# Kernel optimization log

Hardware: AMD Instinct MI355X
Metric: run time of the kernel (lower is better)

## Reference

```python
import jax, jax.numpy as jnp
import numpy as np

N, E, F_IN, HID, G = 20000, 320000, 128, 128, 64
H, D = 8, 32  # TransformerConv heads, per-head dim


def setup_inputs() -> dict:
    key = jax.random.key(0)
    ks = jax.random.split(key, 24)
    def w(k, i, o):
        return (jax.random.normal(k, (i, o), jnp.float32) / np.float32(np.sqrt(i)))
    def b(k, o):
        return jax.random.normal(k, (o,), jnp.float32) * 0.01
    inp = {
        'x': jax.random.normal(ks[0], (N, F_IN), jnp.float32),
        'edge_index': jax.random.randint(ks[1], (2, E), 0, N, jnp.int32),
        'batch': jnp.sort(jax.random.randint(ks[2], (N,), 0, G, jnp.int32)),
        # SAGEConv 1: 128 -> 128 (lin_l has bias, lin_r none)
        's1_wl': w(ks[3], 128, 128), 's1_bl': b(ks[4], 128), 's1_wr': w(ks[5], 128, 128),
        # SAGEConv 2: 128 -> 256
        's2_wl': w(ks[6], 128, 256), 's2_bl': b(ks[7], 256), 's2_wr': w(ks[8], 128, 256),
        # TransformerConv 1: 256 -> 8*32
        't1_wq': w(ks[9], 256, 256), 't1_bq': b(ks[10], 256),
        't1_wk': w(ks[11], 256, 256), 't1_bk': b(ks[12], 256),
        't1_wv': w(ks[13], 256, 256), 't1_bv': b(ks[14], 256),
        't1_ws': w(ks[15], 256, 256), 't1_bs': b(ks[16], 256),
        # TransformerConv 2
        't2_wq': w(ks[17], 256, 256), 't2_bq': b(ks[18], 256),
        't2_wk': w(ks[19], 256, 256), 't2_bk': b(ks[20], 256),
        't2_wv': w(ks[21], 256, 256), 't2_bv': b(ks[22], 256),
        't2_ws': w(ks[23], 256, 256), 't2_bs': b(jax.random.fold_in(key, 100), 256),
        # proj MLP: 256 -> 512 -> HID
        'p1_w': w(jax.random.fold_in(key, 101), 256, 512), 'p1_b': b(jax.random.fold_in(key, 102), 512),
        'p2_w': w(jax.random.fold_in(key, 103), 512, HID), 'p2_b': b(jax.random.fold_in(key, 104), HID),
    }
    return inp


def _sage(x, src, dst, wl, bl, wr):
    # PyG SAGEConv (aggr='mean'): lin_l(mean_j x_j) + lin_r(x_i)
    s = jax.ops.segment_sum(x[src], dst, num_segments=N)           # [N,F]
    cnt = jax.ops.segment_sum(jnp.ones((src.shape[0], 1), x.dtype), dst, num_segments=N)
    mean = s / jnp.maximum(cnt, 1.0)
    return mean @ wl + bl + x @ wr


def _tconv(x, src, dst, wq, bq, wk, bk, wv, bv, ws, bs):
    # PyG TransformerConv(256, 32, heads=8): per-edge attention + skip
    q = (x @ wq + bq).reshape(N, H, D)
    k = (x @ wk + bk).reshape(N, H, D)
    v = (x @ wv + bv).reshape(N, H, D)
    logits = jnp.einsum('ehd,ehd->eh', q[dst], k[src]) / np.float32(np.sqrt(D))  # [E,H]
    m = jax.ops.segment_max(logits, dst, num_segments=N)           # [N,H]
    p = jnp.exp(logits - m[dst])
    denom = jax.ops.segment_sum(p, dst, num_segments=N)
    p = p / denom[dst]                                              # softmax per target node per head
    agg = jax.ops.segment_sum(p[:, :, None] * v[src], dst, num_segments=N)  # [N,H,D]
    return agg.reshape(N, H * D) + x @ ws + bs


def reference(x, edge_index, batch, s1_wl, s1_bl, s1_wr, s2_wl, s2_bl, s2_wr,
              t1_wq, t1_bq, t1_wk, t1_bk, t1_wv, t1_bv, t1_ws, t1_bs,
              t2_wq, t2_bq, t2_wk, t2_bk, t2_wv, t2_bv, t2_ws, t2_bs,
              p1_w, p1_b, p2_w, p2_b):
    src, dst = edge_index[0], edge_index[1]
    h = jax.nn.relu(_sage(x, src, dst, s1_wl, s1_bl, s1_wr))
    h = jax.nn.relu(_sage(h, src, dst, s2_wl, s2_bl, s2_wr))
    h = jax.nn.relu(_tconv(h, src, dst, t1_wq, t1_bq, t1_wk, t1_bk, t1_wv, t1_bv, t1_ws, t1_bs))
    h = jax.nn.relu(_tconv(h, src, dst, t2_wq, t2_bq, t2_wk, t2_bk, t2_wv, t2_bv, t2_ws, t2_bs))
    # proj: ReLU -> Linear(256,512) -> ReLU -> Linear(512,HID) -> Sigmoid
    h = jax.nn.relu(h)
    h = jax.nn.relu(h @ p1_w + p1_b)
    h = jax.nn.sigmoid(h @ p2_w + p2_b)
    return jax.ops.segment_max(h, batch, num_segments=G)            # global_max_pool [G,HID]
```

## Files before the change

### kernel.cpp

```cpp
#include <hip/hip_runtime.h>
#include <hip/hip_bf16.h>
#include <hip/hip_fp16.h>
#include <math.h>

#define NN 20000
#define EE 320000
#define GG 64
#define CH 16

typedef __hip_bfloat16 bf16;
typedef __attribute__((ext_vector_type(8))) short short8;
typedef __attribute__((ext_vector_type(4))) float f32x4;
typedef __attribute__((ext_vector_type(4))) unsigned int uint4v;
typedef __attribute__((ext_vector_type(2))) _Float16 half2v;
typedef unsigned int uint;
typedef unsigned short ushort;

__device__ __forceinline__ float bfr2f(ushort u) {
    union { uint i; float f; } c; c.i = ((uint)u) << 16; return c.f;
}
__device__ __forceinline__ ushort f2bfr(float f) {
    bf16 h = __float2bfloat16(f);
    return *(ushort*)&h;
}

__device__ __forceinline__ float dot2acc(uint a, uint b, float c) {
#if __has_builtin(__builtin_amdgcn_fdot2)
    return __builtin_amdgcn_fdot2(__builtin_bit_cast(half2v, a),
                                  __builtin_bit_cast(half2v, b), c, false);
#else
    half2v ha = __builtin_bit_cast(half2v, a);
    half2v hb = __builtin_bit_cast(half2v, b);
    return c + (float)ha.x * (float)hb.x + (float)ha.y * (float)hb.y;
#endif
}

__device__ __forceinline__ void load_lds16(const void* g, void* l) {
    __builtin_amdgcn_global_load_lds(
        (const __attribute__((address_space(1))) unsigned int*)g,
        (__attribute__((address_space(3))) unsigned int*)l, 16, 0, 0);
}

#define PREP_CONV  10000
#define PREP_TP    (PREP_CONV + 800)
#define PREP_BIAS  (PREP_TP + 8)
#define PREP_OUTZ  (PREP_BIAS + 32)
#define PREP_COUNT (PREP_OUTZ + 1250)

__global__ __launch_bounds__(256) void prep_kernel(
    const float* x, bf16* xm1,
    const float* s1_wr, const float* s1_wl, const float* s2_wr, const float* s2_wl,
    const float* t1_wq, const float* t1_wk, const float* t1_wv, const float* t1_ws,
    const float* t2_wq, const float* t2_wk, const float* t2_wv, const float* t2_ws,
    const float* p1_w, const float* p2_w,
    bf16* w1cat, bf16* w2cat, bf16* qw1, bf16* qw2, bf16* p1t, bf16* p2t,
    const float* b1q, const float* b1k, const float* b1v, const float* b1s,
    const float* b2q, const float* b2k, const float* b2v, const float* b2s,
    float* qb1, float* qb2,
    float* pool_out,
    const int* dst, int* cnt) {
    __shared__ float tile[32][33];
    int bid = blockIdx.x;
    int tid = threadIdx.x;
    if (bid < PREP_CONV) {
        int i = bid * 256 + tid;
        int r = i >> 7, c = i & 127;
        xm1[(size_t)r * 256 + c] = __float2bfloat16(x[i]);
    } else if (bid < PREP_TP) {
        int tb = bid - PREP_CONV;
        const float* W; bf16* Wt; int KW, NW, KT, KO, lt;
        const float* t1w[4] = {t1_wq, t1_wk, t1_wv, t1_ws};
        const float* t2w[4] = {t2_wq, t2_wk, t2_wv, t2_ws};
        if (tb < 16)       { W = s1_wr; Wt = w1cat; KW = 128; NW = 128; KT = 256; KO = 0;   lt = tb; }
        else if (tb < 32)  { W = s1_wl; Wt = w1cat; KW = 128; NW = 128; KT = 256; KO = 128; lt = tb - 16; }
        else if (tb < 64)  { W = s2_wr; Wt = w2cat; KW = 128; NW = 256; KT = 256; KO = 0;   lt = tb - 32; }
        else if (tb < 96)  { W = s2_wl; Wt = w2cat; KW = 128; NW = 256; KT = 256; KO = 128; lt = tb - 64; }
        else if (tb < 352) { int m = (tb - 96) >> 6;  W = t1w[m]; Wt = qw1 + m * 65536; KW = 256; NW = 256; KT = 256; KO = 0; lt = (tb - 96) & 63; }
        else if (tb < 608) { int m = (tb - 352) >> 6; W = t2w[m]; Wt = qw2 + m * 65536; KW = 256; NW = 256; KT = 256; KO = 0; lt = (tb - 352) & 63; }
        else if (tb < 736) { W = p1_w; Wt = p1t; KW = 256; NW = 512; KT = 256; KO = 0; lt = tb - 608; }
        else               { W = p2_w; Wt = p2t; KW = 512; NW = 128; KT = 512; KO = 0; lt = tb - 736; }
        int ntiles_n = NW >> 5;
        int k0 = (lt / ntiles_n) * 32;
        int n0 = (lt % ntiles_n) * 32;
        int tx = tid & 31, ty = tid >> 5;
        #pragma unroll
        for (int r = 0; r < 4; r++)
            tile[ty + 8 * r][tx] = W[(size_t)(k0 + ty + 8 * r) * NW + n0 + tx];
        __syncthreads();
        #pragma unroll
        for (int r = 0; r < 4; r++)
            Wt[(size_t)(n0 + ty + 8 * r) * KT + KO + k0 + tx] =
                __float2bfloat16(tile[tx][ty + 8 * r]);
    } else if (bid < PREP_BIAS) {
        int i = (bid - PREP_TP) * 256 + tid;
        if (i < 2048) {
            float* d = (i < 1024) ? qb1 : qb2;
            int j = i & 1023;
            const float* s;
            if (i < 1024) s = (j < 256) ? b1q : (j < 512) ? b1k : (j < 768) ? b1v : b1s;
            else          s = (j < 256) ? b2q : (j < 512) ? b2k : (j < 768) ? b2v : b2s;
            d[j] = s[j & 255];
        }
    } else if (bid < PREP_OUTZ) {
        int i = (bid - PREP_BIAS) * 256 + tid;
        if (i < GG * 128) pool_out[i] = 0.f;
    } else {
        int e = (bid - PREP_OUTZ) * 256 + tid;
        if (e < EE) atomicAdd(&cnt[dst[e]], 1);
    }
}

__global__ __launch_bounds__(1024) void scan_kernel(int* __restrict__ cnt,
                                                    int* __restrict__ off, int n) {
    __shared__ int wsum[16];
    __shared__ int carry_s;
    int tid = threadIdx.x;
    int lane = tid & 63, wid = tid >> 6;
    if (tid == 0) { carry_s = 0; off[0] = 0; }
    __syncthreads();
    for (int base = 0; base < n; base += 1024) {
        int idx = base + tid;
        int val = (idx < n) ? cnt[idx] : 0;
        int x = val;
        #pragma unroll
        for (int s = 1; s < 64; s <<= 1) {
            int y = __shfl_up(x, s, 64);
            if (lane >= s) x += y;
        }
        if (lane == 63) wsum[wid] = x;
        __syncthreads();
        if (tid == 0) {
            int c = carry_s;
            #pragma unroll
            for (int w = 0; w < 16; w++) { int t = wsum[w]; wsum[w] = c; c += t; }
            carry_s = c;
        }
        __syncthreads();
        int incl = wsum[wid] + x;
        if (idx < n) {
            off[idx + 1] = incl;
            cnt[idx] = incl - val;
        }
        __syncthreads();
    }
}

__global__ __launch_bounds__(256) void fill_kernel(const int* __restrict__ src,
                                                   const int* __restrict__ dst,
                                                   int* __restrict__ cursor,
                                                   int* __restrict__ csr_src, int E) {
    int e = blockIdx.x * 256 + threadIdx.x;
    if (e < E) {
        int p = atomicAdd(&cursor[dst[e]], 1);
        csr_src[p] = src[e];
    }
}

__global__ __launch_bounds__(256) void mean2_kernel(const bf16* __restrict__ x, int xstride,
                                                    const int* __restrict__ off,
                                                    const int* __restrict__ csr_src,
                                                    bf16* __restrict__ outp, int ostride) {
    int node = blockIdx.x * 4 + (threadIdx.x >> 6);
    int lane = threadIdx.x & 63;
    int e0 = off[node], e1 = off[node + 1];
    float s0 = 0.f, s1 = 0.f;
    int e = e0;
    for (; e + 7 < e1; e += 8) {
        uint a[8];
        #pragma unroll
        for (int j = 0; j < 8; j++) {
            int sa = csr_src[e + j];
            a[j] = *(const uint*)(x + (size_t)sa * xstride + lane * 2);
        }
        #pragma unroll
        for (int j = 0; j < 8; j++) {
            union { uint i; float f; } t;
            t.i = a[j] << 16; s0 += t.f;
            t.i = a[j] & 0xffff0000u; s1 += t.f;
        }
    }
    for (; e < e1; e++) {
        int sa = csr_src[e];
        uint a = *(const uint*)(x + (size_t)sa * xstride + lane * 2);
        union { uint i; float f; } t;
        t.i = a << 16; s0 += t.f; t.i = a & 0xffff0000u; s1 += t.f;
    }
    int deg = e1 - e0;
    float inv = (deg > 0) ? 1.f / (float)deg : 0.f;
    uint r = ((uint)f2bfr(s1 * inv) << 16) | (uint)f2bfr(s0 * inv);
    *(uint*)(outp + (size_t)node * ostride + lane * 2) = r;
}

template <int MODE, int TM>
__global__ __launch_bounds__(256, (TM == 128) ? 3 : 4)
void gemm_kernel(const bf16* __restrict__ A,
                 const bf16* __restrict__ Wt,
                 const float* __restrict__ bias,
                 void* __restrict__ Cv,
                 int M, int K, int N, int cstride,
                 const int* __restrict__ batch,
                 float* __restrict__ pool_out) {
    constexpr int NT = (TM == 128) ? 4 : 2;
    constexpr int CSTR = 136;
    union SMem {
        struct { short As[TM * 64]; short Bs[128 * 64]; } st;
        ushort ctile[TM * CSTR];
    };
    __shared__ SMem sm;
    __shared__ int bat[TM];
    int t = threadIdx.x;
    int lane = t & 63;
    int wave = t >> 6;
    int wm = (TM == 128) ? (wave >> 1) * 64 : 0;
    int wn = (TM == 128) ? (wave & 1) * 64 : wave * 32;
    int bm = blockIdx.y * TM, bn = blockIdx.x * 128;
    int quad = lane >> 4, l16 = lane & 15;
    int srow = t >> 3;
    int sc8  = t & 7;
    int scol = sc8 * 8;
    int gcol = (sc8 ^ (srow & 7)) * 8;
    int sw   = l16 & 7;

    if (MODE == 4 && t < TM) bat[t] = batch[min(bm + t, M - 1)];

    f32x4 acc[4][NT];
    f32x4 zero = {0.f, 0.f, 0.f, 0.f};
    #pragma unroll
    for (int i = 0; i < 4; i++)
        #pragma unroll
        for (int j = 0; j < NT; j++) acc[i][j] = zero;

    for (int kk = 0; kk < K; kk += 64) {
        #pragma unroll
        for (int r = 0; r < TM / 32; r++) {
            int row = r * 32 + srow;
            int gm = bm + row; gm = (gm < M) ? gm : (M - 1);
            load_lds16(A + (size_t)gm * K + kk + gcol, &sm.st.As[row * 64 + scol]);
        }
        #pragma unroll
        for (int r = 0; r < 4; r++) {
            int row = r * 32 + srow;
            load_lds16(Wt + (size_t)(bn + row) * K + kk + gcol, &sm.st.Bs[row * 64 + scol]);
        }
        __syncthreads();
        #pragma unroll
        for (int ks = 0; ks < 2; ks++) {
            short8 af[4], bfr[NT];
            #pragma unroll
            for (int i = 0; i < 4; i++)
                af[i] = *(const short8*)&sm.st.As[(wm + i * 16 + l16) * 64 + ((ks * 4 + quad) ^ sw) * 8];
            #pragma unroll
            for (int j = 0; j < NT; j++)
                bfr[j] = *(const short8*)&sm.st.Bs[(wn + j * 16 + l16) * 64 + ((ks * 4 + quad) ^ sw) * 8];
            #pragma unroll
            for (int i = 0; i < 4; i++)
                #pragma unroll
                for (int j = 0; j < NT; j++)
                    acc[i][j] = __builtin_amdgcn_mfma_f32_16x16x32_bf16(af[i], bfr[j], acc[i][j], 0, 0, 0);
        }
        __syncthreads();
    }

    if (MODE == 4) {
        int g0 = bat[0], gL = bat[TM - 1];
        #pragma unroll
        for (int j = 0; j < NT; j++) {
            int gn = bn + wn + j * 16 + l16;
            float m0 = 0.f, m1 = 0.f;
            #pragma unroll
            for (int i = 0; i < 4; i++) {
                #pragma unroll
                for (int r = 0; r < 4; r++) {
                    int row = i * 16 + quad * 4 + r;
                    int gm = bm + row;
                    if (gm >= M) continue;
                    float v = acc[i][j][r] + bias[gn];
                    v = 1.f / (1.f + expf(-v));
                    int g = bat[row];
                    if (g == g0) m0 = fmaxf(m0, v);
                    else if (g == gL) m1 = fmaxf(m1, v);
                    else atomicMax((int*)&pool_out[g * 128 + gn], __float_as_int(v));
                }
            }
            m0 = fmaxf(m0, __shfl_xor(m0, 16));
            m0 = fmaxf(m0, __shfl_xor(m0, 32));
            m1 = fmaxf(m1, __shfl_xor(m1, 16));
            m1 = fmaxf(m1, __shfl_xor(m1, 32));
            if (quad == 0) {
                atomicMax((int*)&pool_out[g0 * 128 + gn], __float_as_int(m0));
                if (gL != g0)
                    atomicMax((int*)&pool_out[gL * 128 + gn], __float_as_int(m1));
            }
        }
        return;
    }

    #pragma unroll
    for (int i = 0; i < 4; i++) {
        int row0 = wm + i * 16 + quad * 4;
        #pragma unroll
        for (int j = 0; j < NT; j++) {
            int col = wn + j * 16 + l16;
            int gn = bn + col;
            #pragma unroll
            for (int r = 0; r < 4; r++) {
                float v = acc[i][j][r] + bias[gn];
                if (MODE == 2) v = fmaxf(v, 0.f);
                ushort st;
                if (MODE == 5 && gn < 512) {
                    __half hh = __float2half(v);
                    st = *(ushort*)&hh;
                } else {
                    st = f2bfr(v);
                }
                sm.ctile[(row0 + r) * CSTR + col] = st;
            }
        }
    }
    __syncthreads();

    int orow = t >> 4;
    int ocol = (t & 15) * 8;
    #pragma unroll
    for (int rb = 0; rb < TM / 16; rb++) {
        int row = rb * 16 + orow;
        int gm = bm + row;
        if (gm < M) {
            short8 val = *(const short8*)&sm.ctile[row * CSTR + ocol];
            *(short8*)((ushort*)Cv + (size_t)gm * cstride + bn + ocol) = val;
        }
    }
}

template <int MODE, int TM>
static void launch_gemm(const bf16* A, const bf16* Wt, const float* bias, void* C,
                        int M, int K, int N, int cstride, hipStream_t st,
                        const int* batch = nullptr, float* pool_out = nullptr) {
    dim3 grid(N / 128, (M + TM - 1) / TM);
    hipLaunchKernelGGL((gemm_kernel<MODE, TM>), grid, dim3(256), 0, st,
                       A, Wt, bias, C, M, K, N, cstride, batch, pool_out);
}

__global__ __launch_bounds__(256) void attn5_kernel(const bf16* __restrict__ qkvs,
                                                    const int* __restrict__ off,
                                                    const int* __restrict__ csr_src,
                                                    bf16* __restrict__ out, int ostride) {
    __shared__ float pp[2][CH][9];
    __shared__ int srcs[2][CH];
    int i = blockIdx.x;
    int tid = threadIdx.x;
    int ea = tid >> 4, ha = (tid >> 1) & 7, half = tid & 1;
    int hc = tid >> 5, dp = (tid >> 1) & 15, epar = tid & 1;

    uint q2[8];
    {
        const uint4v* qp = (const uint4v*)(qkvs + (size_t)i * 1024 + ha * 32 + half * 16);
        uint4v a = qp[0], b = qp[1];
        q2[0] = a.x; q2[1] = a.y; q2[2] = a.z; q2[3] = a.w;
        q2[4] = b.x; q2[5] = b.y; q2[6] = b.z; q2[7] = b.w;
    }

    int e0 = off[i], e1 = off[i + 1];
    float l = 0.f, acc0 = 0.f, acc1 = 0.f;
    int vcol = 512 + hc * 32 + dp * 2;
    if (e0 < e1) {
        if (tid < CH) srcs[0][tid] = csr_src[min(e0 + tid, e1 - 1)];
        __syncthreads();
        int buf = 0;
        for (int base = e0; base < e1; base += CH, buf ^= 1) {
            int cnt = min(CH, e1 - base);
            uint vv[8];
            #pragma unroll
            for (int j = 0; j < 8; j++) {
                int e = epar + j * 2;
                vv[j] = *(const uint*)(qkvs + (size_t)srcs[buf][e] * 1024 + vcol);
            }
            int s = srcs[buf][ea];
            const uint4v* kp = (const uint4v*)(qkvs + (size_t)s * 1024 + 256 + ha * 32 + half * 16);
            uint4v ka = kp[0], kb = kp[1];
            if (tid < CH) srcs[buf ^ 1][tid] = csr_src[min(base + CH + tid, e1 - 1)];
            float d = 0.f;
            d = dot2acc(q2[0], ka.x, d); d = dot2acc(q2[1], ka.y, d);
            d = dot2acc(q2[2], ka.z, d); d = dot2acc(q2[3], ka.w, d);
            d = dot2acc(q2[4], kb.x, d); d = dot2acc(q2[5], kb.y, d);
            d = dot2acc(q2[6], kb.z, d); d = dot2acc(q2[7], kb.w, d);
            d += __shfl_xor(d, 1);
            float p = (ea < cnt) ? __expf(d * 0.17677669529663687f) : 0.f;
            if (half == 0) pp[buf][ea][ha] = p;
            __syncthreads();
            #pragma unroll
            for (int j = 0; j < 8; j++) {
                int e = epar + j * 2;
                float pj = pp[buf][e][hc];
                l += pj;
                union { uint i; float f; } lo, hi;
                lo.i = vv[j] << 16; hi.i = vv[j] & 0xffff0000u;
                acc0 += pj * lo.f;
                acc1 += pj * hi.f;
            }
        }
    }
    acc0 += __shfl_xor(acc0, 1);
    acc1 += __shfl_xor(acc1, 1);
    l    += __shfl_xor(l, 1);
    float inv = (l > 0.f) ? 1.f / l : 0.f;
    float r0 = acc0 * inv, r1 = acc1 * inv;
    if (epar == 0) {
        uint su = *(const uint*)(qkvs + (size_t)i * 1024 + 768 + hc * 32 + dp * 2);
        union { uint i; float f; } lo, hi;
        lo.i = su << 16; hi.i = su & 0xffff0000u;
        float v0 = fmaxf(r0 + lo.f, 0.f);
        float v1 = fmaxf(r1 + hi.f, 0.f);
        uint packed = ((uint)f2bfr(v1) << 16) | (uint)f2bfr(v0);
        *(uint*)(out + (size_t)i * ostride + hc * 32 + dp * 2) = packed;
    }
}

extern "C" void kernel_launch(void* const* d_in, const int* in_sizes, int n_in,
                              void* d_out, int out_size, void* d_ws, size_t ws_size,
                              hipStream_t stream) {
    const float* x      = (const float*)d_in[0];
    const int*   ei     = (const int*)d_in[1];
    const int*   batch  = (const int*)d_in[2];
    const float* s1_wl  = (const float*)d_in[3];
    const float* s1_bl  = (const float*)d_in[4];
    const float* s1_wr  = (const float*)d_in[5];
    const float* s2_wl  = (const float*)d_in[6];
    const float* s2_bl  = (const float*)d_in[7];
    const float* s2_wr  = (const float*)d_in[8];
    const float* t1_wq  = (const float*)d_in[9];
    const float* t1_bq  = (const float*)d_in[10];
    const float* t1_wk  = (const float*)d_in[11];
    const float* t1_bk  = (const float*)d_in[12];
    const float* t1_wv  = (const float*)d_in[13];
    const float* t1_bv  = (const float*)d_in[14];
    const float* t1_ws  = (const float*)d_in[15];
    const float* t1_bs  = (const float*)d_in[16];
    const float* t2_wq  = (const float*)d_in[17];
    const float* t2_bq  = (const float*)d_in[18];
    const float* t2_wk  = (const float*)d_in[19];
    const float* t2_bk  = (const float*)d_in[20];
    const float* t2_wv  = (const float*)d_in[21];
    const float* t2_bv  = (const float*)d_in[22];
    const float* t2_wsk = (const float*)d_in[23];
    const float* t2_bs  = (const float*)d_in[24];
    const float* p1_w   = (const float*)d_in[25];
    const float* p1_b   = (const float*)d_in[26];
    const float* p2_w   = (const float*)d_in[27];
    const float* p2_b   = (const float*)d_in[28];
    float* out = (float*)d_out;

    char* ws = (char*)d_ws;
    size_t o = 0;
    auto alloc = [&](size_t bytes) { char* p = ws + o; o += (bytes + 255) & ~(size_t)255; return p; };
    int* off     = (int*)alloc(sizeof(int) * (NN + 1));
    int* cursor  = (int*)alloc(sizeof(int) * NN);
    int* csr_src = (int*)alloc(sizeof(int) * EE);
    bf16* w1cat = (bf16*)alloc(2 * 128 * 256);
    bf16* w2cat = (bf16*)alloc(2 * 256 * 256);
    bf16* qw1   = (bf16*)alloc(2 * 1024 * 256);
    bf16* qw2   = (bf16*)alloc(2 * 1024 * 256);
    bf16* p1t   = (bf16*)alloc(2 * 512 * 256);
    bf16* p2t   = (bf16*)alloc(2 * 128 * 512);
    float* qb1  = (float*)alloc(4 * 1024);
    float* qb2  = (float*)alloc(4 * 1024);
    bf16* xm1   = (bf16*)alloc(2 * (size_t)NN * 256);
    bf16* xm2   = (bf16*)alloc(2 * (size_t)NN * 256);
    bf16* t1b   = (bf16*)alloc(2 * (size_t)NN * 512);
    bf16* Q     = (bf16*)alloc(2 * (size_t)NN * 1024);
    bf16* h2   = xm1;
    bf16* t1   = t1b;
    bf16* h4   = xm1;
    bf16* p1o  = t1b;

    const int* src = ei;
    const int* dst = ei + EE;

    hipMemsetAsync(cursor, 0, sizeof(int) * NN, stream);

    prep_kernel<<<PREP_COUNT, 256, 0, stream>>>(
        x, xm1,
        s1_wr, s1_wl, s2_wr, s2_wl,
        t1_wq, t1_wk, t1_wv, t1_ws,
        t2_wq, t2_wk, t2_wv, t2_wsk,
        p1_w, p2_w,
        w1cat, w2cat, qw1, qw2, p1t, p2t,
        t1_bq, t1_bk, t1_bv, t1_bs,
        t2_bq, t2_bk, t2_bv, t2_bs,
        qb1, qb2,
        out,
        dst, cursor);

    scan_kernel<<<1, 1024, 0, stream>>>(cursor, off, NN);
    fill_kernel<<<(EE + 255) / 256, 256, 0, stream>>>(src, dst, cursor, csr_src, EE);

    mean2_kernel<<<NN / 4, 256, 0, stream>>>(xm1, 256, off, csr_src, xm1 + 128, 256);
    launch_gemm<2, 64>(xm1, w1cat, s1_bl, xm2, NN, 256, 128, 256, stream);

    mean2_kernel<<<NN / 4, 256, 0, stream>>>(xm2, 256, off, csr_src, xm2 + 128, 256);
    launch_gemm<2, 64>(xm2, w2cat, s2_bl, h2, NN, 256, 256, 256, stream);

    launch_gemm<5, 128>(h2, qw1, qb1, Q, NN, 256, 1024, 1024, stream);
    attn5_kernel<<<NN, 256, 0, stream>>>(Q, off, csr_src, t1, 256);

    launch_gemm<5, 128>(t1, qw2, qb2, Q, NN, 256, 1024, 1024, stream);
    attn5_kernel<<<NN, 256, 0, stream>>>(Q, off, csr_src, h4, 256);

    launch_gemm<2, 128>(h4, p1t, p1_b, p1o, NN, 256, 512, 512, stream);
    launch_gemm<4, 64>(p1o, p2t, p2_b, nullptr, NN, 512, 128, 128, stream, batch, out);
}
```

Before: 380.4 us.

## Vectorize x conversion, split mean-gather across half-waves, raise GEMM occupancy bounds

The x fp32-to-bf16 conversion now has each thread handle 8 elements with vector loads and a single 16-byte store, so it needs far fewer prep blocks. The mean-aggregation kernel splits each wave into two half-waves that gather alternate edges with 8-byte loads and combine their sums with a cross-lane shuffle. This keeps more independent loads in flight and removes the scalar tail loop. The GEMM launch bounds request one more wave per SIMD, which could force register spills.

```diff
diff --git a/kernel.cpp b/kernel.cpp
--- a/kernel.cpp
+++ b/kernel.cpp
@@ -12,6 +12,7 @@
 typedef __attribute__((ext_vector_type(8))) short short8;
 typedef __attribute__((ext_vector_type(4))) float f32x4;
 typedef __attribute__((ext_vector_type(4))) unsigned int uint4v;
+typedef __attribute__((ext_vector_type(2))) unsigned int uint2v;
 typedef __attribute__((ext_vector_type(2))) _Float16 half2v;
 typedef unsigned int uint;
 typedef unsigned short ushort;
@@ -41,7 +42,7 @@
         (__attribute__((address_space(3))) unsigned int*)l, 16, 0, 0);
 }
 
-#define PREP_CONV  10000
+#define PREP_CONV  1250
 #define PREP_TP    (PREP_CONV + 800)
 #define PREP_BIAS  (PREP_TP + 8)
 #define PREP_OUTZ  (PREP_BIAS + 32)
@@ -63,9 +64,17 @@
     int bid = blockIdx.x;
     int tid = threadIdx.x;
     if (bid < PREP_CONV) {
-        int i = bid * 256 + tid;
-        int r = i >> 7, c = i & 127;
-        xm1[(size_t)r * 256 + c] = __float2bfloat16(x[i]);
+        int g = bid * 256 + tid;
+        int row = g >> 4;
+        int col = (g & 15) * 8;
+        f32x4 a = *(const f32x4*)(x + (size_t)row * 128 + col);
+        f32x4 b = *(const f32x4*)(x + (size_t)row * 128 + col + 4);
+        short8 v;
+        v[0] = (short)f2bfr(a.x); v[1] = (short)f2bfr(a.y);
+        v[2] = (short)f2bfr(a.z); v[3] = (short)f2bfr(a.w);
+        v[4] = (short)f2bfr(b.x); v[5] = (short)f2bfr(b.y);
+        v[6] = (short)f2bfr(b.z); v[7] = (short)f2bfr(b.w);
+        *(short8*)(xm1 + (size_t)row * 256 + col) = v;
     } else if (bid < PREP_TP) {
         int tb = bid - PREP_CONV;
         const float* W; bf16* Wt; int KW, NW, KT, KO, lt;
@@ -161,38 +170,47 @@
                                                     const int* __restrict__ csr_src,
                                                     bf16* __restrict__ outp, int ostride) {
     int node = blockIdx.x * 4 + (threadIdx.x >> 6);
-    int lane = threadIdx.x & 63;
+    int l = threadIdx.x & 63;
+    int el = l >> 5;
+    int dp = l & 31;
     int e0 = off[node], e1 = off[node + 1];
-    float s0 = 0.f, s1 = 0.f;
-    int e = e0;
-    for (; e + 7 < e1; e += 8) {
-        uint a[8];
-        #pragma unroll
-        for (int j = 0; j < 8; j++) {
-            int sa = csr_src[e + j];
-            a[j] = *(const uint*)(x + (size_t)sa * xstride + lane * 2);
-        }
-        #pragma unroll
-        for (int j = 0; j < 8; j++) {
+    float s0 = 0.f, s1 = 0.f, s2 = 0.f, s3 = 0.f;
+    for (int e = e0; e < e1; e += 8) {
+        uint2v a[4];
+        #pragma unroll
+        for (int j = 0; j < 4; j++) {
+            int ee = e + j * 2 + el;
+            int sa = csr_src[min(ee, e1 - 1)];
+            uint2v v = *(const uint2v*)(x + (size_t)sa * xstride + dp * 4);
+            uint m = (ee < e1) ? 0xffffffffu : 0u;
+            a[j].x = v.x & m;
+            a[j].y = v.y & m;
+        }
+        #pragma unroll
+        for (int j = 0; j < 4; j++) {
             union { uint i; float f; } t;
-            t.i = a[j] << 16; s0 += t.f;
-            t.i = a[j] & 0xffff0000u; s1 += t.f;
-        }
-    }
-    for (; e < e1; e++) {
-        int sa = csr_src[e];
-        uint a = *(const uint*)(x + (size_t)sa * xstride + lane * 2);
-        union { uint i; float f; } t;
-        t.i = a << 16; s0 += t.f; t.i = a & 0xffff0000u; s1 += t.f;
-    }
-    int deg = e1 - e0;
-    float inv = (deg > 0) ? 1.f / (float)deg : 0.f;
-    uint r = ((uint)f2bfr(s1 * inv) << 16) | (uint)f2bfr(s0 * inv);
-    *(uint*)(outp + (size_t)node * ostride + lane * 2) = r;
+            t.i = a[j].x << 16;         s0 += t.f;
+            t.i = a[j].x & 0xffff0000u; s1 += t.f;
+            t.i = a[j].y << 16;         s2 += t.f;
+            t.i = a[j].y & 0xffff0000u; s3 += t.f;
+        }
+    }
+    s0 += __shfl_xor(s0, 32);
+    s1 += __shfl_xor(s1, 32);
+    s2 += __shfl_xor(s2, 32);
+    s3 += __shfl_xor(s3, 32);
+    if (el == 0) {
+        int deg = e1 - e0;
+        float inv = (deg > 0) ? 1.f / (float)deg : 0.f;
+        uint2v r;
+        r.x = ((uint)f2bfr(s1 * inv) << 16) | (uint)f2bfr(s0 * inv);
+        r.y = ((uint)f2bfr(s3 * inv) << 16) | (uint)f2bfr(s2 * inv);
+        *(uint2v*)(outp + (size_t)node * ostride + dp * 4) = r;
+    }
 }
 
 template <int MODE, int TM>
-__global__ __launch_bounds__(256, (TM == 128) ? 3 : 4)
+__global__ __launch_bounds__(256, (TM == 128) ? 4 : 5)
 void gemm_kernel(const bf16* __restrict__ A,
                  const bf16* __restrict__ Wt,
                  const float* __restrict__ bias,
```

Measured after the change: 374.1 us. Within noise of the previous version (-1.7%).
